# Kernel optimization log

Measured on AMD Instinct MI355X. Metric: run time of the kernel, lower is better.

Reference implementation:

```python
import jax, jax.numpy as jnp
import numpy as np

N_NODES = 10000
N_EDGES = 320000
OBS_DIM = 30
ACT_DIM = 4
HID = 128


def setup_inputs() -> dict:
    key = jax.random.key(0)
    ks = jax.random.split(key, 16)

    def lin(k, fan_in, fan_out):
        s = 1.0 / np.sqrt(fan_in)
        kw, kb = jax.random.split(k)
        w = jax.random.uniform(kw, (fan_in, fan_out), jnp.float32, -s, s)
        b = jax.random.uniform(kb, (fan_out,), jnp.float32, -s, s)
        return w, b

    obs = jax.random.normal(ks[0], (N_NODES, OBS_DIM), jnp.float32)
    action = jax.random.normal(ks[1], (N_NODES, ACT_DIM), jnp.float32)
    edge_index = jax.random.randint(ks[2], (2, N_EDGES), 0, N_NODES, jnp.int64)

    w_g1, b_g1 = lin(ks[3], OBS_DIM + ACT_DIM, HID)
    w_g2, b_g2 = lin(ks[4], HID, HID)
    w_q1a, b_q1a = lin(ks[5], HID, HID)
    w_q1b, b_q1b = lin(ks[6], HID, 1)
    w_q2a, b_q2a = lin(ks[7], HID, HID)
    w_q2b, b_q2b = lin(ks[8], HID, 1)

    return dict(obs=obs, action=action, edge_index=edge_index,
                w_g1=w_g1, b_g1=b_g1, w_g2=w_g2, b_g2=b_g2,
                w_q1a=w_q1a, b_q1a=b_q1a, w_q1b=w_q1b, b_q1b=b_q1b,
                w_q2a=w_q2a, b_q2a=b_q2a, w_q2b=w_q2b, b_q2b=b_q2b)


def gcn_conv(x, w, b, src, dst, deg_inv_sqrt, n):
    xw = x @ w                                      # [N, Fout] small GEMM
    norm = deg_inv_sqrt[src] * deg_inv_sqrt[dst]    # [E'] edge norm
    msg = xw[src] * norm[:, None]                   # gather + scale, [E', Fout]
    out = jax.ops.segment_sum(msg, dst, num_segments=n)  # scatter-add
    return out + b


def reference(obs, action, edge_index,
              w_g1, b_g1, w_g2, b_g2,
              w_q1a, b_q1a, w_q1b, b_q1b,
              w_q2a, b_q2a, w_q2b, b_q2b):
    n = obs.shape[0]
    loops = jnp.arange(n, dtype=edge_index.dtype)
    src = jnp.concatenate([edge_index[0], loops])   # add self-loops
    dst = jnp.concatenate([edge_index[1], loops])

    deg = jnp.zeros((n,), jnp.float32).at[dst].add(1.0)
    deg_inv_sqrt = jnp.where(deg > 0, jax.lax.rsqrt(jnp.maximum(deg, 1.0)), 0.0)

    x = jnp.concatenate([obs, action], axis=1)
    x = jax.nn.relu(gcn_conv(x, w_g1, b_g1, src, dst, deg_inv_sqrt, n))
    x = jax.nn.relu(gcn_conv(x, w_g2, b_g2, src, dst, deg_inv_sqrt, n))

    q1 = jax.nn.relu(x @ w_q1a + b_q1a) @ w_q1b + b_q1b
    q2 = jax.nn.relu(x @ w_q2a + b_q2a) @ w_q2b + b_q2b
    return (q1, q2)
```

## Files before the change

### kernel.cpp

```cpp
#include <hip/hip_runtime.h>

#define N_NODES 10000
#define N_EDGES 320000
#define OBS_DIM 30
#define ACT_DIM 4
#define HID 128
#define ELL_W 96
#define SENT N_NODES


__global__ __launch_bounds__(256) void k_init(int* __restrict__ cnt,
                                              float* __restrict__ xpad,
                                              float* __restrict__ y2,
                                              const float* __restrict__ obs,
                                              const float* __restrict__ act) {
    int i = blockIdx.x * 256 + threadIdx.x;
    if (i < (N_NODES + 1) * 16) {
        int row = i >> 4, sub = i & 15;
        float4 v = make_float4(0.f, 0.f, 0.f, 0.f);
        if (row < N_NODES) {
            float* vv = &v.x;
#pragma unroll
            for (int k = 0; k < 4; ++k) {
                int c = sub * 4 + k;
                if (c < OBS_DIM) vv[k] = obs[row * OBS_DIM + c];
                else if (c < OBS_DIM + ACT_DIM) vv[k] = act[row * ACT_DIM + (c - OBS_DIM)];
            }
        }
        ((float4*)xpad)[i] = v;
    }
    if (i <= N_NODES) cnt[i] = 0;
    if (i < HID / 4)
        ((float4*)(y2 + (size_t)SENT * HID))[i] = make_float4(0.f, 0.f, 0.f, 0.f);
}


__global__ __launch_bounds__(256) void k_build(const int4* __restrict__ src4,
                                               const int4* __restrict__ dst4,
                                               int* __restrict__ cnt,
                                               int* __restrict__ col) {
    int i = blockIdx.x * 256 + threadIdx.x;
    if (i < N_EDGES / 4) {
        int4 s = src4[i];
        int4 d = dst4[i];
        int p;
        p = atomicAdd(&cnt[d.x], 1); col[d.x * ELL_W + p] = s.x;
        p = atomicAdd(&cnt[d.y], 1); col[d.y * ELL_W + p] = s.y;
        p = atomicAdd(&cnt[d.z], 1); col[d.z * ELL_W + p] = s.z;
        p = atomicAdd(&cnt[d.w], 1); col[d.w * ELL_W + p] = s.w;
    }
}


__global__ __launch_bounds__(512) void k_agg1_gemm1(const float4* __restrict__ x4,
                                                    const int* __restrict__ cnt,
                                                    const int* __restrict__ col,
                                                    const float* __restrict__ W1,
                                                    const float* __restrict__ b1,
                                                    float* __restrict__ dis,
                                                    float* __restrict__ h1) {
    __shared__ float ws[34 * 128];
    __shared__ float zs[8][64];
    int t = threadIdx.x;
    {
        float4* wsp = (float4*)ws;
        const float4* Wp = (const float4*)W1;
        for (int i = t; i < 34 * 128 / 4; i += 512) wsp[i] = Wp[i];
    }
    __syncthreads();
    int wave = t >> 6, lane = t & 63, g = lane >> 4, sub = lane & 15;
    int node = blockIdx.x * 8 + wave;
    int deg = cnt[node];
    float di = rsqrtf((float)(deg + 1));
    const int* cp = col + node * ELL_W;
    float4 a = make_float4(0.f, 0.f, 0.f, 0.f);
    if (g == 0) {
        float4 xv = x4[node * 16 + sub];
        a.x = di * xv.x; a.y = di * xv.y; a.z = di * xv.z; a.w = di * xv.w;
    }
    for (int e = 0; e < deg; e += 8) {
        int s0 = e + g, s1 = e + 4 + g;
        int j0 = (s0 < deg) ? cp[s0] : SENT;
        int j1 = (s1 < deg) ? cp[s1] : SENT;
        float d0 = rsqrtf((float)(cnt[j0] + 1));
        float d1 = rsqrtf((float)(cnt[j1] + 1));
        float4 v0 = x4[j0 * 16 + sub];
        float4 v1 = x4[j1 * 16 + sub];
        a.x += d0 * v0.x + d1 * v1.x;
        a.y += d0 * v0.y + d1 * v1.y;
        a.z += d0 * v0.z + d1 * v1.z;
        a.w += d0 * v0.w + d1 * v1.w;
    }
    a.x += __shfl_xor(a.x, 16); a.x += __shfl_xor(a.x, 32);
    a.y += __shfl_xor(a.y, 16); a.y += __shfl_xor(a.y, 32);
    a.z += __shfl_xor(a.z, 16); a.z += __shfl_xor(a.z, 32);
    a.w += __shfl_xor(a.w, 16); a.w += __shfl_xor(a.w, 32);
    if (g == 0) {
        float4 z;
        z.x = di * a.x; z.y = di * a.y; z.z = di * a.z; z.w = di * a.w;
        *(float4*)&zs[wave][sub * 4] = z;
    }
    if (lane == 0) dis[node] = di;
    float h0 = b1[lane], h64 = b1[lane + 64];
#pragma unroll
    for (int k = 0; k < 34; ++k) {
        float zk = zs[wave][k];
        h0 += zk * ws[k * 128 + lane];
        h64 += zk * ws[k * 128 + 64 + lane];
    }
    h1[node * HID + lane] = fmaxf(h0, 0.0f);
    h1[node * HID + 64 + lane] = fmaxf(h64, 0.0f);
}


__global__ __launch_bounds__(256) void k_gemm128(const float* __restrict__ x,
                                                 const float* __restrict__ W,
                                                 const float* __restrict__ dis,
                                                 float* __restrict__ y) {
    __shared__ float xs[16 * 128];
    __shared__ float ws[32 * 128];
    int t = threadIdx.x;
    int row0 = blockIdx.x * 16;
    {
        float4* xsp = (float4*)xs;
        const float4* xp = (const float4*)(x + row0 * 128);
        for (int i = t; i < 512; i += 256) xsp[i] = xp[i];
    }
    int c = t & 127, half = t >> 7;
    float acc[8] = {0, 0, 0, 0, 0, 0, 0, 0};
    for (int ch = 0; ch < 4; ++ch) {
        __syncthreads();
        {
            float4* wsp = (float4*)ws;
            const float4* Wp = (const float4*)(W + ch * 4096);
            for (int i = t; i < 1024; i += 256) wsp[i] = Wp[i];
        }
        __syncthreads();
        for (int k = 0; k < 32; ++k) {
            float wv = ws[k * 128 + c];
#pragma unroll
            for (int r = 0; r < 8; ++r)
                acc[r] += xs[(half * 8 + r) * 128 + ch * 32 + k] * wv;
        }
    }
#pragma unroll
    for (int r = 0; r < 8; ++r) {
        int row = row0 + half * 8 + r;
        y[row * 128 + c] = dis[row] * acc[r];
    }
}


__global__ __launch_bounds__(256) void k_agg2(const float4* __restrict__ y4,
                                              const int* __restrict__ cnt,
                                              const int* __restrict__ col,
                                              const float* __restrict__ dis,
                                              const float4* __restrict__ bias4,
                                              float4* __restrict__ out4) {
    int t = threadIdx.x;
    int wave = t >> 6, lane = t & 63, half = lane >> 5, sub = lane & 31;
    int node = blockIdx.x * 4 + wave;
    if (node >= N_NODES) return;
    int deg = cnt[node];
    const int* cp = col + node * ELL_W;
    float4 a = make_float4(0.f, 0.f, 0.f, 0.f);
    if (!half) a = y4[node * 32 + sub];
    for (int e = 0; e < deg; e += 8) {
        int s0 = e + half, s1 = e + 2 + half, s2 = e + 4 + half, s3 = e + 6 + half;
        int j0 = (s0 < deg) ? cp[s0] : SENT;
        int j1 = (s1 < deg) ? cp[s1] : SENT;
        int j2 = (s2 < deg) ? cp[s2] : SENT;
        int j3 = (s3 < deg) ? cp[s3] : SENT;
        float4 v0 = y4[j0 * 32 + sub];
        float4 v1 = y4[j1 * 32 + sub];
        float4 v2 = y4[j2 * 32 + sub];
        float4 v3 = y4[j3 * 32 + sub];
        a.x += (v0.x + v1.x) + (v2.x + v3.x);
        a.y += (v0.y + v1.y) + (v2.y + v3.y);
        a.z += (v0.z + v1.z) + (v2.z + v3.z);
        a.w += (v0.w + v1.w) + (v2.w + v3.w);
    }
    a.x += __shfl_xor(a.x, 32);
    a.y += __shfl_xor(a.y, 32);
    a.z += __shfl_xor(a.z, 32);
    a.w += __shfl_xor(a.w, 32);
    if (!half) {
        float dn = dis[node];
        float4 b = bias4[sub];
        float4 r;
        r.x = fmaxf(dn * a.x + b.x, 0.0f);
        r.y = fmaxf(dn * a.y + b.y, 0.0f);
        r.z = fmaxf(dn * a.z + b.z, 0.0f);
        r.w = fmaxf(dn * a.w + b.w, 0.0f);
        out4[node * 32 + sub] = r;
    }
}


__global__ __launch_bounds__(256) void k_heads(const float* __restrict__ x,
                                               const float* __restrict__ W1, const float* __restrict__ B1,
                                               const float* __restrict__ w1b, const float* __restrict__ b1b,
                                               const float* __restrict__ W2, const float* __restrict__ B2,
                                               const float* __restrict__ w2b, const float* __restrict__ b2b,
                                               float* __restrict__ q1, float* __restrict__ q2) {
    __shared__ float xs[16 * 128];
    __shared__ float w1s[32 * 128];
    __shared__ float w2s[32 * 128];
    __shared__ float part1[4][8];
    __shared__ float part2[4][8];
    int t = threadIdx.x;
    int row0 = blockIdx.x * 16;
    {
        float4* xsp = (float4*)xs;
        const float4* xp = (const float4*)(x + row0 * 128);
        for (int i = t; i < 512; i += 256) xsp[i] = xp[i];
    }
    int c = t & 127, half = t >> 7;
    float a1[8] = {0, 0, 0, 0, 0, 0, 0, 0};
    float a2[8] = {0, 0, 0, 0, 0, 0, 0, 0};
    for (int ch = 0; ch < 4; ++ch) {
        __syncthreads();
        {
            float4* w1p = (float4*)w1s;
            float4* w2p = (float4*)w2s;
            const float4* W1p = (const float4*)(W1 + ch * 4096);
            const float4* W2p = (const float4*)(W2 + ch * 4096);
            for (int i = t; i < 1024; i += 256) {
                w1p[i] = W1p[i];
                w2p[i] = W2p[i];
            }
        }
        __syncthreads();
        for (int k = 0; k < 32; ++k) {
            float wv1 = w1s[k * 128 + c];
            float wv2 = w2s[k * 128 + c];
#pragma unroll
            for (int r = 0; r < 8; ++r) {
                float xv = xs[(half * 8 + r) * 128 + ch * 32 + k];
                a1[r] += xv * wv1;
                a2[r] += xv * wv2;
            }
        }
    }
    float bb1 = B1[c], bb2 = B2[c];
    float v1 = w1b[c], v2 = w2b[c];
    float s1[8], s2[8];
#pragma unroll
    for (int r = 0; r < 8; ++r) {
        float h1 = fmaxf(a1[r] + bb1, 0.0f);
        float h2 = fmaxf(a2[r] + bb2, 0.0f);
        s1[r] = h1 * v1;
        s2[r] = h2 * v2;
    }
#pragma unroll
    for (int off = 1; off < 64; off <<= 1) {
#pragma unroll
        for (int r = 0; r < 8; ++r) {
            s1[r] += __shfl_xor(s1[r], off);
            s2[r] += __shfl_xor(s2[r], off);
        }
    }
    int wave = t >> 6, lane = t & 63;
    if (lane == 0) {
#pragma unroll
        for (int r = 0; r < 8; ++r) {
            part1[wave][r] = s1[r];
            part2[wave][r] = s2[r];
        }
    }
    __syncthreads();
    if (t < 16) {
        int hf = t >> 3, r = t & 7;
        int row = row0 + hf * 8 + r;
        q1[row] = part1[hf * 2][r] + part1[hf * 2 + 1][r] + b1b[0];
        q2[row] = part2[hf * 2][r] + part2[hf * 2 + 1][r] + b2b[0];
    }
}

extern "C" void kernel_launch(void* const* d_in, const int* in_sizes, int n_in,
                              void* d_out, int out_size, void* d_ws, size_t ws_size,
                              hipStream_t stream) {
    (void)in_sizes; (void)n_in; (void)out_size; (void)ws_size;
    const float* obs  = (const float*)d_in[0];
    const float* act  = (const float*)d_in[1];
    const int*   ei   = (const int*)d_in[2];
    const int*   src  = ei;
    const int*   dst  = ei + N_EDGES;
    const float* w_g1 = (const float*)d_in[3];
    const float* b_g1 = (const float*)d_in[4];
    const float* w_g2 = (const float*)d_in[5];
    const float* b_g2 = (const float*)d_in[6];
    const float* w_q1a = (const float*)d_in[7];
    const float* b_q1a = (const float*)d_in[8];
    const float* w_q1b = (const float*)d_in[9];
    const float* b_q1b = (const float*)d_in[10];
    const float* w_q2a = (const float*)d_in[11];
    const float* b_q2a = (const float*)d_in[12];
    const float* w_q2b = (const float*)d_in[13];
    const float* b_q2b = (const float*)d_in[14];
    float* out = (float*)d_out;

    char* ws = (char*)d_ws;
    size_t off = 0;
    auto alloc = [&](size_t bytes) {
        void* p = ws + off;
        off = (off + bytes + 255) & ~(size_t)255;
        return p;
    };
    int*   cnt  = (int*)alloc((N_NODES + 1) * 4);
    float* dis  = (float*)alloc(N_NODES * 4);
    int*   col  = (int*)alloc((size_t)N_NODES * ELL_W * 4);
    float* xpad = (float*)alloc((size_t)(N_NODES + 1) * 64 * 4);
    float* h1b  = (float*)alloc((size_t)N_NODES * HID * 4);
    float* y2b  = (float*)alloc((size_t)(N_NODES + 1) * HID * 4);
    float* h2b  = (float*)alloc((size_t)N_NODES * HID * 4);

    k_init<<<((N_NODES + 1) * 16 + 255) / 256, 256, 0, stream>>>(cnt, xpad, y2b, obs, act);
    k_build<<<(N_EDGES / 4 + 255) / 256, 256, 0, stream>>>(
        (const int4*)src, (const int4*)dst, cnt, col);

    k_agg1_gemm1<<<1250, 512, 0, stream>>>((const float4*)xpad, cnt, col,
                                           w_g1, b_g1, dis, h1b);
    k_gemm128<<<625, 256, 0, stream>>>(h1b, w_g2, dis, y2b);
    k_agg2<<<2500, 256, 0, stream>>>((const float4*)y2b, cnt, col, dis,
                                     (const float4*)b_g2, (float4*)h2b);
    k_heads<<<625, 256, 0, stream>>>(h2b, w_q1a, b_q1a, w_q1b, b_q1b,
                                     w_q2a, b_q2a, w_q2b, b_q2b,
                                     out, out + N_NODES);
}
```

Baseline: 107.8 us.

## Reorder layer-2 as aggregate-then-GEMM and fuse into one kernel

```diff
diff --git a/kernel.cpp b/kernel.cpp
--- a/kernel.cpp
+++ b/kernel.cpp
@@ -11,7 +11,7 @@
 
 __global__ __launch_bounds__(256) void k_init(int* __restrict__ cnt,
                                               float* __restrict__ xpad,
-                                              float* __restrict__ y2,
+                                              float* __restrict__ ph1,
                                               const float* __restrict__ obs,
                                               const float* __restrict__ act) {
     int i = blockIdx.x * 256 + threadIdx.x;
@@ -31,7 +31,7 @@
     }
     if (i <= N_NODES) cnt[i] = 0;
     if (i < HID / 4)
-        ((float4*)(y2 + (size_t)SENT * HID))[i] = make_float4(0.f, 0.f, 0.f, 0.f);
+        ((float4*)(ph1 + (size_t)SENT * HID))[i] = make_float4(0.f, 0.f, 0.f, 0.f);
 }
 
 
@@ -52,20 +52,19 @@
 }
 
 
-__global__ __launch_bounds__(512) void k_agg1_gemm1(const float4* __restrict__ x4,
-                                                    const int* __restrict__ cnt,
-                                                    const int* __restrict__ col,
-                                                    const float* __restrict__ W1,
-                                                    const float* __restrict__ b1,
-                                                    float* __restrict__ dis,
-                                                    float* __restrict__ h1) {
-    __shared__ float ws[34 * 128];
+__global__ __launch_bounds__(512) void k_l1(const float4* __restrict__ x4,
+                                            const int* __restrict__ cnt,
+                                            const int* __restrict__ col,
+                                            const float* __restrict__ W1,
+                                            const float* __restrict__ b1,
+                                            float* __restrict__ ph1) {
+    __shared__ float w1s[34 * 128];
     __shared__ float zs[8][64];
     int t = threadIdx.x;
     {
-        float4* wsp = (float4*)ws;
+        float4* wsp = (float4*)w1s;
         const float4* Wp = (const float4*)W1;
-        for (int i = t; i < 34 * 128 / 4; i += 512) wsp[i] = Wp[i];
+        for (int i = t; i < 1088; i += 512) wsp[i] = Wp[i];
     }
     __syncthreads();
     int wave = t >> 6, lane = t & 63, g = lane >> 4, sub = lane & 15;
@@ -100,100 +99,81 @@
         z.x = di * a.x; z.y = di * a.y; z.z = di * a.z; z.w = di * a.w;
         *(float4*)&zs[wave][sub * 4] = z;
     }
-    if (lane == 0) dis[node] = di;
     float h0 = b1[lane], h64 = b1[lane + 64];
 #pragma unroll
     for (int k = 0; k < 34; ++k) {
         float zk = zs[wave][k];
-        h0 += zk * ws[k * 128 + lane];
-        h64 += zk * ws[k * 128 + 64 + lane];
-    }
-    h1[node * HID + lane] = fmaxf(h0, 0.0f);
-    h1[node * HID + 64 + lane] = fmaxf(h64, 0.0f);
-}
-
-
-__global__ __launch_bounds__(256) void k_gemm128(const float* __restrict__ x,
-                                                 const float* __restrict__ W,
-                                                 const float* __restrict__ dis,
-                                                 float* __restrict__ y) {
-    __shared__ float xs[16 * 128];
-    __shared__ float ws[32 * 128];
+        h0 += zk * w1s[k * 128 + lane];
+        h64 += zk * w1s[k * 128 + 64 + lane];
+    }
+    ph1[node * HID + lane] = di * fmaxf(h0, 0.0f);
+    ph1[node * HID + 64 + lane] = di * fmaxf(h64, 0.0f);
+}
+
+
+__global__ __launch_bounds__(512) void k_aggW2(const float4* __restrict__ ph14,
+                                               const int* __restrict__ cnt,
+                                               const int* __restrict__ col,
+                                               const float* __restrict__ W2,
+                                               const float* __restrict__ b2,
+                                               float* __restrict__ h2) {
+    __shared__ float2 w2p[128 * 64];
+    __shared__ float zs[16][128];
     int t = threadIdx.x;
-    int row0 = blockIdx.x * 16;
-    {
-        float4* xsp = (float4*)xs;
-        const float4* xp = (const float4*)(x + row0 * 128);
-        for (int i = t; i < 512; i += 256) xsp[i] = xp[i];
-    }
-    int c = t & 127, half = t >> 7;
-    float acc[8] = {0, 0, 0, 0, 0, 0, 0, 0};
-    for (int ch = 0; ch < 4; ++ch) {
-        __syncthreads();
-        {
-            float4* wsp = (float4*)ws;
-            const float4* Wp = (const float4*)(W + ch * 4096);
-            for (int i = t; i < 1024; i += 256) wsp[i] = Wp[i];
-        }
-        __syncthreads();
-        for (int k = 0; k < 32; ++k) {
-            float wv = ws[k * 128 + c];
-#pragma unroll
-            for (int r = 0; r < 8; ++r)
-                acc[r] += xs[(half * 8 + r) * 128 + ch * 32 + k] * wv;
-        }
-    }
-#pragma unroll
-    for (int r = 0; r < 8; ++r) {
-        int row = row0 + half * 8 + r;
-        y[row * 128 + c] = dis[row] * acc[r];
-    }
-}
-
-
-__global__ __launch_bounds__(256) void k_agg2(const float4* __restrict__ y4,
-                                              const int* __restrict__ cnt,
-                                              const int* __restrict__ col,
-                                              const float* __restrict__ dis,
-                                              const float4* __restrict__ bias4,
-                                              float4* __restrict__ out4) {
-    int t = threadIdx.x;
+    for (int i = t; i < 128 * 64; i += 512) {
+        int k = i >> 6, c = i & 63;
+        w2p[i] = make_float2(W2[k * 128 + c], W2[k * 128 + 64 + c]);
+    }
+    __syncthreads();
     int wave = t >> 6, lane = t & 63, half = lane >> 5, sub = lane & 31;
-    int node = blockIdx.x * 4 + wave;
-    if (node >= N_NODES) return;
-    int deg = cnt[node];
-    const int* cp = col + node * ELL_W;
-    float4 a = make_float4(0.f, 0.f, 0.f, 0.f);
-    if (!half) a = y4[node * 32 + sub];
-    for (int e = 0; e < deg; e += 8) {
-        int s0 = e + half, s1 = e + 2 + half, s2 = e + 4 + half, s3 = e + 6 + half;
-        int j0 = (s0 < deg) ? cp[s0] : SENT;
-        int j1 = (s1 < deg) ? cp[s1] : SENT;
-        int j2 = (s2 < deg) ? cp[s2] : SENT;
-        int j3 = (s3 < deg) ? cp[s3] : SENT;
-        float4 v0 = y4[j0 * 32 + sub];
-        float4 v1 = y4[j1 * 32 + sub];
-        float4 v2 = y4[j2 * 32 + sub];
-        float4 v3 = y4[j3 * 32 + sub];
-        a.x += (v0.x + v1.x) + (v2.x + v3.x);
-        a.y += (v0.y + v1.y) + (v2.y + v3.y);
-        a.z += (v0.z + v1.z) + (v2.z + v3.z);
-        a.w += (v0.w + v1.w) + (v2.w + v3.w);
-    }
-    a.x += __shfl_xor(a.x, 32);
-    a.y += __shfl_xor(a.y, 32);
-    a.z += __shfl_xor(a.z, 32);
-    a.w += __shfl_xor(a.w, 32);
-    if (!half) {
-        float dn = dis[node];
-        float4 b = bias4[sub];
-        float4 r;
-        r.x = fmaxf(dn * a.x + b.x, 0.0f);
-        r.y = fmaxf(dn * a.y + b.y, 0.0f);
-        r.z = fmaxf(dn * a.z + b.z, 0.0f);
-        r.w = fmaxf(dn * a.w + b.w, 0.0f);
-        out4[node * 32 + sub] = r;
-    }
+    int node0 = blockIdx.x * 16 + wave * 2;
+    float di[2];
+#pragma unroll
+    for (int n = 0; n < 2; ++n) {
+        int node = node0 + n;
+        int deg = cnt[node];
+        di[n] = rsqrtf((float)(deg + 1));
+        const int* cp = col + node * ELL_W;
+        float4 a = make_float4(0.f, 0.f, 0.f, 0.f);
+        if (!half) a = ph14[node * 32 + sub];
+        for (int e = 0; e < deg; e += 8) {
+            int s0 = e + half, s1 = e + 2 + half, s2 = e + 4 + half, s3 = e + 6 + half;
+            int j0 = (s0 < deg) ? cp[s0] : SENT;
+            int j1 = (s1 < deg) ? cp[s1] : SENT;
+            int j2 = (s2 < deg) ? cp[s2] : SENT;
+            int j3 = (s3 < deg) ? cp[s3] : SENT;
+            float4 v0 = ph14[j0 * 32 + sub];
+            float4 v1 = ph14[j1 * 32 + sub];
+            float4 v2 = ph14[j2 * 32 + sub];
+            float4 v3 = ph14[j3 * 32 + sub];
+            a.x += (v0.x + v1.x) + (v2.x + v3.x);
+            a.y += (v0.y + v1.y) + (v2.y + v3.y);
+            a.z += (v0.z + v1.z) + (v2.z + v3.z);
+            a.w += (v0.w + v1.w) + (v2.w + v3.w);
+        }
+        a.x += __shfl_xor(a.x, 32);
+        a.y += __shfl_xor(a.y, 32);
+        a.z += __shfl_xor(a.z, 32);
+        a.w += __shfl_xor(a.w, 32);
+        if (!half) *(float4*)&zs[wave * 2 + n][sub * 4] = a;
+    }
+    float a00 = 0.f, a01 = 0.f, a10 = 0.f, a11 = 0.f;
+    for (int k4 = 0; k4 < 32; ++k4) {
+        float4 s0 = *(float4*)&zs[wave * 2][k4 * 4];
+        float4 s1 = *(float4*)&zs[wave * 2 + 1][k4 * 4];
+#pragma unroll
+        for (int j = 0; j < 4; ++j) {
+            float2 w = w2p[(k4 * 4 + j) * 64 + lane];
+            float s0j = (&s0.x)[j], s1j = (&s1.x)[j];
+            a00 += s0j * w.x; a01 += s0j * w.y;
+            a10 += s1j * w.x; a11 += s1j * w.y;
+        }
+    }
+    float bb0 = b2[lane], bb64 = b2[lane + 64];
+    h2[(node0 + 0) * HID + lane]      = fmaxf(di[0] * a00 + bb0, 0.0f);
+    h2[(node0 + 0) * HID + 64 + lane] = fmaxf(di[0] * a01 + bb64, 0.0f);
+    h2[(node0 + 1) * HID + lane]      = fmaxf(di[1] * a10 + bb0, 0.0f);
+    h2[(node0 + 1) * HID + 64 + lane] = fmaxf(di[1] * a11 + bb64, 0.0f);
 }
 
 
@@ -247,10 +227,8 @@
     float s1[8], s2[8];
 #pragma unroll
     for (int r = 0; r < 8; ++r) {
-        float h1 = fmaxf(a1[r] + bb1, 0.0f);
-        float h2 = fmaxf(a2[r] + bb2, 0.0f);
-        s1[r] = h1 * v1;
-        s2[r] = h2 * v2;
+        s1[r] = fmaxf(a1[r] + bb1, 0.0f) * v1;
+        s2[r] = fmaxf(a2[r] + bb2, 0.0f) * v2;
     }
 #pragma unroll
     for (int off = 1; off < 64; off <<= 1) {
@@ -308,22 +286,16 @@
         return p;
     };
     int*   cnt  = (int*)alloc((N_NODES + 1) * 4);
-    float* dis  = (float*)alloc(N_NODES * 4);
     int*   col  = (int*)alloc((size_t)N_NODES * ELL_W * 4);
     float* xpad = (float*)alloc((size_t)(N_NODES + 1) * 64 * 4);
-    float* h1b  = (float*)alloc((size_t)N_NODES * HID * 4);
-    float* y2b  = (float*)alloc((size_t)(N_NODES + 1) * HID * 4);
+    float* ph1  = (float*)alloc((size_t)(N_NODES + 1) * HID * 4);
     float* h2b  = (float*)alloc((size_t)N_NODES * HID * 4);
 
-    k_init<<<((N_NODES + 1) * 16 + 255) / 256, 256, 0, stream>>>(cnt, xpad, y2b, obs, act);
+    k_init<<<((N_NODES + 1) * 16 + 255) / 256, 256, 0, stream>>>(cnt, xpad, ph1, obs, act);
     k_build<<<(N_EDGES / 4 + 255) / 256, 256, 0, stream>>>(
         (const int4*)src, (const int4*)dst, cnt, col);
-
-    k_agg1_gemm1<<<1250, 512, 0, stream>>>((const float4*)xpad, cnt, col,
-                                           w_g1, b_g1, dis, h1b);
-    k_gemm128<<<625, 256, 0, stream>>>(h1b, w_g2, dis, y2b);
-    k_agg2<<<2500, 256, 0, stream>>>((const float4*)y2b, cnt, col, dis,
-                                     (const float4*)b_g2, (float4*)h2b);
+    k_l1<<<1250, 512, 0, stream>>>((const float4*)xpad, cnt, col, w_g1, b_g1, ph1);
+    k_aggW2<<<625, 512, 0, stream>>>((const float4*)ph1, cnt, col, w_g2, b_g2, h2b);
     k_heads<<<625, 256, 0, stream>>>(h2b, w_q1a, b_q1a, w_q1b, b_q1b,
                                      w_q2a, b_q2a, w_q2b, b_q2b,
                                      out, out + N_NODES);
```

Result: slower. 115.3 us (+7.0%).
